# Optimization experiments

Measured on AMD Instinct MI355X. Metric: run time of the kernel, lower is better.

Reference implementation:

```python
import jax, jax.numpy as jnp
import numpy as np

B, S, H, R, N = 8, 4096, 1024, 128, 256
A_LOGIT_INIT = 6.906754778648554      # logit(0.999)
DELTA_LOG_INIT = 0.5413248546129181   # log(exp(1.0) - 1.0), softplus^-1(1.0)


def setup_inputs() -> dict:
    key = jax.random.key(0)
    ks = jax.random.split(key, 6)
    x = jax.random.normal(ks[0], (B, S, H), dtype=jnp.float32)
    state0 = jnp.zeros((B, N), dtype=jnp.float32)
    in_basis = jax.random.normal(ks[1], (R, H), dtype=jnp.float32) / np.sqrt(H)
    q_select = jax.random.normal(ks[2], (N, R), dtype=jnp.float32) / np.sqrt(R)
    k_select = jax.random.normal(ks[3], (N, R), dtype=jnp.float32) / np.sqrt(R)
    v_input = jax.random.normal(ks[4], (N, R), dtype=jnp.float32) / np.sqrt(R)
    out_proj = jax.random.normal(ks[5], (H, N), dtype=jnp.float32) / np.sqrt(N)
    a_logit = jnp.full((N,), A_LOGIT_INIT, dtype=jnp.float32)
    delta_log = jnp.full((N,), DELTA_LOG_INIT, dtype=jnp.float32)
    return {"x": x, "state0": state0, "in_basis": in_basis, "q_select": q_select,
            "k_select": k_select, "v_input": v_input, "out_proj": out_proj,
            "a_logit": a_logit, "delta_log": delta_log}


def reference(x, state0, in_basis, q_select, k_select, v_input, out_proj,
              a_logit, delta_log):
    # Projections (all timesteps at once; equivalent to per-step F.linear)
    z = jnp.einsum('bsh,rh->bsr', x, in_basis)          # [B,S,R]
    b = jnp.einsum('bsr,nr->bsn', z, k_select)          # [B,S,N]
    c = jnp.einsum('bsr,nr->bsn', z, q_select)          # [B,S,N]
    v = jnp.einsum('bsr,nr->bsn', z, v_input)           # [B,S,N]

    a = jax.nn.sigmoid(a_logit)                         # [N]
    delta = jax.nn.softplus(delta_log)                  # [N]
    u = delta * (b * v)                                 # [B,S,N] driving input

    # Diagonal linear recurrence: s_t = a * s_{t-1} + u_t ; y_t = c_t * s_t
    u_t = jnp.swapaxes(u, 0, 1)                         # [S,B,N]
    c_t = jnp.swapaxes(c, 0, 1)                         # [S,B,N]

    def step(s, inp):
        u_i, c_i = inp
        s = a * s + u_i
        return s, c_i * s

    final_state, ys = jax.lax.scan(step, state0, (u_t, c_t))  # ys: [S,B,N]
    out = jnp.einsum('sbn,hn->bsh', ys, out_proj)       # [B,S,H]
    return out, final_state
```

## Files before the change

### kernel.cpp

```cpp
#include <hip/hip_runtime.h>
#include <math.h>

#define Bb 8
#define Ss 4096
#define Hh 1024
#define Rr 128
#define Nn 256
#define Mm (Bb*Ss)
#define LCH 128
#define NCHK (Ss/LCH)

typedef __attribute__((ext_vector_type(8))) short bf16x8;
typedef __attribute__((ext_vector_type(4))) float f32x4;

__device__ __forceinline__ float sigmoidf_(float x) { return 1.0f / (1.0f + expf(-x)); }
__device__ __forceinline__ float softplusf_(float x) { return log1pf(expf(x)); }

__device__ __forceinline__ unsigned short f2b(float f) {
    union { float f; unsigned int u; } v; v.f = f;
    return (unsigned short)((v.u + 0x7fffu + ((v.u >> 16) & 1u)) >> 16);
}
__device__ __forceinline__ float b2f(unsigned short h) {
    union { unsigned int u; float f; } v; v.u = ((unsigned int)h) << 16;
    return v.f;
}

__device__ __forceinline__ void gl_lds16(const void* g, void* l) {
    __builtin_amdgcn_global_load_lds(
        (const __attribute__((address_space(1))) void*)g,
        (__attribute__((address_space(3))) void*)l, 16, 0, 0);
}


__global__ __launch_bounds__(256)
void cast_w(const float* __restrict__ s0, const float* __restrict__ s1,
            const float* __restrict__ s2, const float* __restrict__ s3,
            const float* __restrict__ s4,
            unsigned short* __restrict__ d0, unsigned short* __restrict__ d1,
            unsigned short* __restrict__ d2, unsigned short* __restrict__ d3,
            unsigned short* __restrict__ d4)
{
    const int i = blockIdx.x * 256 + threadIdx.x;
    if (i < 131072)      d0[i] = f2b(s0[i]);
    else if (i < 163840) d1[i - 131072] = f2b(s1[i - 131072]);
    else if (i < 196608) d2[i - 163840] = f2b(s2[i - 163840]);
    else if (i < 229376) d3[i - 196608] = f2b(s3[i - 196608]);
    else                 d4[i - 229376] = f2b(s4[i - 229376]);
}

__global__ __launch_bounds__(256)
void g1_fused(const float* __restrict__ X, const unsigned short* __restrict__ IB,
              unsigned short* __restrict__ Z)
{
    __shared__ __align__(16) unsigned short As[2][64 * 32];
    __shared__ __align__(16) unsigned short Bs[2][128 * 32];
    const int tid = threadIdx.x;
    const int wave = tid >> 6, lane = tid & 63;
    const int m0 = blockIdx.x * 64;
    const int wm = (wave & 1) * 32, wn = (wave >> 1) * 64;
    const int quad = lane >> 4, lm = lane & 15;
    const int srow = lane >> 2;
    const int skoff = (((lane & 3) ^ ((srow >> 1) & 3)) << 3);
    const int qsw = ((quad ^ ((lm >> 1) & 3)) << 3);
    const int arow = tid >> 3;
    const int akf = (tid & 7) * 4;
    const int awoff = ((((tid & 7) >> 1) ^ ((arow >> 1) & 3)) << 3) + (tid & 1) * 4;

    f32x4 acc[2][4] = {};
    float4 va[2];

#pragma unroll
    for (int q = 0; q < 2; ++q)
        va[q] = *(const float4*)(X + (size_t)(m0 + q * 32 + arow) * Hh + akf);
    gl_lds16(IB + (size_t)(2 * wave * 16 + srow) * Hh + skoff, &Bs[0][wave * 1024]);
    gl_lds16(IB + (size_t)((2 * wave + 1) * 16 + srow) * Hh + skoff, &Bs[0][wave * 1024 + 512]);
#pragma unroll
    for (int q = 0; q < 2; ++q) {
        uint2 o;
        o.x = (unsigned)f2b(va[q].x) | ((unsigned)f2b(va[q].y) << 16);
        o.y = (unsigned)f2b(va[q].z) | ((unsigned)f2b(va[q].w) << 16);
        *(uint2*)&As[0][(q * 32 + arow) * 32 + awoff] = o;
    }
    __syncthreads();

    int cur = 0;
    for (int k0 = 0; k0 < Hh; k0 += 32) {
        const int nxt = cur ^ 1;
        const bool more = (k0 + 32) < Hh;
        if (more) {
            gl_lds16(IB + (size_t)(2 * wave * 16 + srow) * Hh + k0 + 32 + skoff, &Bs[nxt][wave * 1024]);
            gl_lds16(IB + (size_t)((2 * wave + 1) * 16 + srow) * Hh + k0 + 32 + skoff, &Bs[nxt][wave * 1024 + 512]);
#pragma unroll
            for (int q = 0; q < 2; ++q)
                va[q] = *(const float4*)(X + (size_t)(m0 + q * 32 + arow) * Hh + k0 + 32 + akf);
        }
        bf16x8 af[2], bfv[4];
#pragma unroll
        for (int i = 0; i < 2; ++i)
            af[i] = *(const bf16x8*)&As[cur][(wm + i * 16 + lm) * 32 + qsw];
#pragma unroll
        for (int j = 0; j < 4; ++j)
            bfv[j] = *(const bf16x8*)&Bs[cur][(wn + j * 16 + lm) * 32 + qsw];
#pragma unroll
        for (int i = 0; i < 2; ++i)
#pragma unroll
            for (int j = 0; j < 4; ++j)
                acc[i][j] = __builtin_amdgcn_mfma_f32_16x16x32_bf16(af[i], bfv[j], acc[i][j], 0, 0, 0);
        if (more) {
#pragma unroll
            for (int q = 0; q < 2; ++q) {
                uint2 o;
                o.x = (unsigned)f2b(va[q].x) | ((unsigned)f2b(va[q].y) << 16);
                o.y = (unsigned)f2b(va[q].z) | ((unsigned)f2b(va[q].w) << 16);
                *(uint2*)&As[nxt][(q * 32 + arow) * 32 + awoff] = o;
            }
        }
        __syncthreads();
        cur = nxt;
    }

#pragma unroll
    for (int i = 0; i < 2; ++i) {
        const int rbase = m0 + wm + i * 16 + quad * 4;
#pragma unroll
        for (int j = 0; j < 4; ++j) {
            const int col = wn + j * 16 + lm;
#pragma unroll
            for (int r = 0; r < 4; ++r)
                Z[(size_t)(rbase + r) * Rr + col] = f2b(acc[i][j][r]);
        }
    }
}

__device__ __forceinline__ void proj_stage(const unsigned short* Zm, const unsigned short* Kw,
                                           const unsigned short* Qw, const unsigned short* Vw,
                                           char* bb, int m0, int n0, int k0,
                                           int wave, int srow, int skoff)
{
    unsigned short* zs = (unsigned short*)bb;
    unsigned short* ks = (unsigned short*)(bb + 8192);
    unsigned short* qs = (unsigned short*)(bb + 12288);
    unsigned short* vs = (unsigned short*)(bb + 16384);
    gl_lds16(Zm + (size_t)(m0 + 2 * wave * 16 + srow) * Rr + k0 + skoff, &zs[wave * 1024]);
    gl_lds16(Zm + (size_t)(m0 + (2 * wave + 1) * 16 + srow) * Rr + k0 + skoff, &zs[wave * 1024 + 512]);
    gl_lds16(Kw + (size_t)(n0 + wave * 16 + srow) * Rr + k0 + skoff, &ks[wave * 512]);
    gl_lds16(Qw + (size_t)(n0 + wave * 16 + srow) * Rr + k0 + skoff, &qs[wave * 512]);
    gl_lds16(Vw + (size_t)(n0 + wave * 16 + srow) * Rr + k0 + skoff, &vs[wave * 512]);
}

__global__ __launch_bounds__(256)
void proj_mfma(const unsigned short* __restrict__ Zm, const unsigned short* __restrict__ Kw,
               const unsigned short* __restrict__ Qw, const unsigned short* __restrict__ Vw,
               const float* __restrict__ delta_log, const float* __restrict__ a_logit,
               unsigned short* __restrict__ U, unsigned short* __restrict__ C,
               float* __restrict__ Pout)
{
    __shared__ __align__(16) char smem[41984];
    float* uL = (float*)smem;
    float* pcomb = (float*)(smem + 40960);

    const int tid = threadIdx.x;
    const int wave = tid >> 6, lane = tid & 63;
    const int m0 = blockIdx.x * 128, n0 = blockIdx.y * 64;
    const int wm = (wave & 1) * 64, wn = (wave >> 1) * 32;
    const int quad = lane >> 4, lm = lane & 15;
    const int srow = lane >> 2;
    const int skoff = (((lane & 3) ^ ((srow >> 1) & 3)) << 3);
    const int qsw = ((quad ^ ((lm >> 1) & 3)) << 3);

    f32x4 aB[4][2] = {}, aC[4][2] = {}, aV[4][2] = {};

    proj_stage(Zm, Kw, Qw, Vw, smem, m0, n0, 0, wave, srow, skoff);
    __syncthreads();

    int cur = 0;
    for (int p = 0; p < 4; ++p) {
        if (p < 3)
            proj_stage(Zm, Kw, Qw, Vw, smem + (cur ^ 1) * 20480, m0, n0,
                       (p + 1) * 32, wave, srow, skoff);
        const unsigned short* zsc = (const unsigned short*)(smem + cur * 20480);
        const unsigned short* ksc = zsc + 4096;
        const unsigned short* qsc = zsc + 6144;
        const unsigned short* vsc = zsc + 8192;
        bf16x8 zf[4], wf[2];
#pragma unroll
        for (int i = 0; i < 4; ++i)
            zf[i] = *(const bf16x8*)&zsc[(wm + i * 16 + lm) * 32 + qsw];
#pragma unroll
        for (int j = 0; j < 2; ++j)
            wf[j] = *(const bf16x8*)&ksc[(wn + j * 16 + lm) * 32 + qsw];
#pragma unroll
        for (int i = 0; i < 4; ++i)
#pragma unroll
            for (int j = 0; j < 2; ++j)
                aB[i][j] = __builtin_amdgcn_mfma_f32_16x16x32_bf16(zf[i], wf[j], aB[i][j], 0, 0, 0);
#pragma unroll
        for (int j = 0; j < 2; ++j)
            wf[j] = *(const bf16x8*)&qsc[(wn + j * 16 + lm) * 32 + qsw];
#pragma unroll
        for (int i = 0; i < 4; ++i)
#pragma unroll
            for (int j = 0; j < 2; ++j)
                aC[i][j] = __builtin_amdgcn_mfma_f32_16x16x32_bf16(zf[i], wf[j], aC[i][j], 0, 0, 0);
#pragma unroll
        for (int j = 0; j < 2; ++j)
            wf[j] = *(const bf16x8*)&vsc[(wn + j * 16 + lm) * 32 + qsw];
#pragma unroll
        for (int i = 0; i < 4; ++i)
#pragma unroll
            for (int j = 0; j < 2; ++j)
                aV[i][j] = __builtin_amdgcn_mfma_f32_16x16x32_bf16(zf[i], wf[j], aV[i][j], 0, 0, 0);
        __syncthreads();
        cur ^= 1;
    }

    float dl[2];
#pragma unroll
    for (int j = 0; j < 2; ++j)
        dl[j] = softplusf_(delta_log[n0 + wn + j * 16 + lm]);

#pragma unroll
    for (int i = 0; i < 4; ++i) {
        const int lrow = wm + i * 16 + quad * 4;
        const int rbase = m0 + lrow;
#pragma unroll
        for (int j = 0; j < 2; ++j) {
            const int col = wn + j * 16 + lm;
            const int gcol = n0 + col;
#pragma unroll
            for (int r = 0; r < 4; ++r) {
                const float uval = dl[j] * aB[i][j][r] * aV[i][j][r];
                const size_t idx = (size_t)(rbase + r) * Nn + gcol;
                U[idx] = f2b(uval);
                C[idx] = f2b(aC[i][j][r]);
                uL[(lrow + r) * 66 + col] = uval;
            }
        }
    }
    __syncthreads();

    const int colp = tid & 63, seg = tid >> 6;
    const float a = sigmoidf_(a_logit[n0 + colp]);
    float l = 0.0f;
#pragma unroll 8
    for (int r = 0; r < 32; ++r)
        l = fmaf(a, l, uL[(seg * 32 + r) * 66 + colp]);
    pcomb[seg * 64 + colp] = l;
    __syncthreads();
    if (tid < 64) {
        float a32 = a;
#pragma unroll
        for (int i = 0; i < 5; ++i) a32 *= a32;
        const float Pv = ((pcomb[tid] * a32 + pcomb[64 + tid]) * a32
                          + pcomb[128 + tid]) * a32 + pcomb[192 + tid];
        Pout[(size_t)blockIdx.x * Nn + n0 + tid] = Pv;
    }
}

__global__ __launch_bounds__(256)
void scan_mid(const float* __restrict__ P, const float* __restrict__ state0,
              const float* __restrict__ a_logit,
              float* __restrict__ start, float* __restrict__ final_state)
{
    const int g = blockIdx.x * blockDim.x + threadIdx.x;
    const int n = g & (Nn - 1);
    const int b = g >> 8;
    const float a = sigmoidf_(a_logit[n]);
    float aL = a;
#pragma unroll
    for (int i = 0; i < 7; ++i) aL *= aL;
    float s = state0[g];
#pragma unroll
    for (int ch = 0; ch < NCHK; ++ch) {
        const size_t idx = ((size_t)(b * NCHK + ch)) * Nn + n;
        start[idx] = s;
        s = fmaf(aL, s, P[idx]);
    }
    final_state[g] = s;
}

__global__ __launch_bounds__(512, 4)
void scan_g4_fused(const unsigned short* __restrict__ U, const unsigned short* __restrict__ C,
                   const float* __restrict__ start, const float* __restrict__ a_logit,
                   const unsigned short* __restrict__ OB, float* __restrict__ Out)
{
    __shared__ __align__(16) unsigned short ys[128 * 256];
    __shared__ __align__(16) unsigned short Bs[2][128 * 32];
    const int tid = threadIdx.x;
    const int wave = tid >> 6, lane = tid & 63;
    const int hbase = blockIdx.x * 512;
    const int m0 = blockIdx.y * 128;
    const int bidx = m0 >> 12;
    const int ch = (m0 & (Ss - 1)) >> 7;
    const int quad = lane >> 4, lm = lane & 15;
    const int srow = lane >> 2;
    const int skoff = (((lane & 3) ^ ((srow >> 1) & 3)) << 3);
    const int qsw = ((quad ^ ((lm >> 1) & 3)) << 3);

    if (tid < 128) {
        const int n = tid * 2;
        const float a0 = sigmoidf_(a_logit[n]);
        const float a1 = sigmoidf_(a_logit[n + 1]);
        const size_t sb = ((size_t)(bidx * NCHK + ch)) * Nn + n;
        float s0 = start[sb], s1 = start[sb + 1];
        size_t gb = ((size_t)m0) * Nn + n;
        const int slot = n >> 3;
        const int e = n & 7;
#pragma unroll 8
        for (int t = 0; t < LCH; ++t) {
            const unsigned uu = *(const unsigned*)(U + gb);
            const unsigned cc = *(const unsigned*)(C + gb);
            s0 = fmaf(a0, s0, b2f((unsigned short)uu));
            s1 = fmaf(a1, s1, b2f((unsigned short)(uu >> 16)));
            const float y0 = b2f((unsigned short)cc) * s0;
            const float y1 = b2f((unsigned short)(cc >> 16)) * s1;
            *(unsigned*)&ys[t * 256 + (((slot ^ (t & 7)) << 3) + e)] =
                (unsigned)f2b(y0) | ((unsigned)f2b(y1) << 16);
            gb += Nn;
        }
    } else if (wave >= 4) {
#pragma unroll
        for (int q = 0; q < 2; ++q) {
            const int reg = 2 * (wave - 4) + q;
            gl_lds16(OB + (size_t)(hbase + reg * 16 + srow) * Nn + skoff, &Bs[0][reg * 512]);
        }
    }
    __syncthreads();

    const int wm = (wave & 1) * 64, wn = (wave >> 1) * 32;
    f32x4 acc[4][2];

    for (int kk = 0; kk < 32; ++kk) {
        const int buf = kk & 1;
        if ((kk & 7) == 0) {
#pragma unroll
            for (int i = 0; i < 4; ++i)
#pragma unroll
                for (int j = 0; j < 2; ++j)
                    acc[i][j] = (f32x4){0.f, 0.f, 0.f, 0.f};
        }
        if (kk + 1 < 32) {
            const int n0g = hbase + ((kk + 1) >> 3) * 128;
            const int k0n = ((kk + 1) & 7) * 32;
            gl_lds16(OB + (size_t)(n0g + wave * 16 + srow) * Nn + k0n + skoff,
                     &Bs[buf ^ 1][wave * 512]);
        }
        const int k0 = (kk & 7) * 32;
        const int c8 = (k0 >> 3) + quad;
        bf16x8 af[4], bfv[2];
#pragma unroll
        for (int i = 0; i < 4; ++i) {
            const int r = wm + i * 16 + lm;
            af[i] = *(const bf16x8*)&ys[r * 256 + ((c8 ^ (r & 7)) << 3)];
        }
#pragma unroll
        for (int j = 0; j < 2; ++j)
            bfv[j] = *(const bf16x8*)&Bs[buf][(wn + j * 16 + lm) * 32 + qsw];
#pragma unroll
        for (int i = 0; i < 4; ++i)
#pragma unroll
            for (int j = 0; j < 2; ++j)
                acc[i][j] = __builtin_amdgcn_mfma_f32_16x16x32_bf16(af[i], bfv[j], acc[i][j], 0, 0, 0);
        if ((kk & 7) == 7) {
            const int n0g = hbase + (kk >> 3) * 128;
#pragma unroll
            for (int i = 0; i < 4; ++i) {
                const int rbase = m0 + wm + i * 16 + quad * 4;
#pragma unroll
                for (int j = 0; j < 2; ++j) {
                    const int col = n0g + wn + j * 16 + lm;
#pragma unroll
                    for (int r = 0; r < 4; ++r)
                        Out[(size_t)(rbase + r) * Hh + col] = acc[i][j][r];
                }
            }
        }
        __syncthreads();
    }
}

extern "C" void kernel_launch(void* const* d_in, const int* in_sizes, int n_in,
                              void* d_out, int out_size, void* d_ws, size_t ws_size,
                              hipStream_t stream)
{
    const float* x         = (const float*)d_in[0];
    const float* state0    = (const float*)d_in[1];
    const float* in_basis  = (const float*)d_in[2];
    const float* q_select  = (const float*)d_in[3];
    const float* k_select  = (const float*)d_in[4];
    const float* v_input   = (const float*)d_in[5];
    const float* out_proj  = (const float*)d_in[6];
    const float* a_logit   = (const float*)d_in[7];
    const float* delta_log = (const float*)d_in[8];

    float* out = (float*)d_out;
    float* final_state = out + (size_t)Mm * Hh;

    char* ws = (char*)d_ws;
    unsigned short* u  = (unsigned short*)ws;
    unsigned short* c  = (unsigned short*)(ws + 16777216);
    unsigned short* zb = (unsigned short*)(ws + 33554432);
    unsigned short* ib = (unsigned short*)(ws + 41943040);
    unsigned short* kb = (unsigned short*)(ws + 42205184);
    unsigned short* qb = (unsigned short*)(ws + 42270720);
    unsigned short* vb = (unsigned short*)(ws + 42336256);
    unsigned short* ob = (unsigned short*)(ws + 42401792);
    float* P  = (float*)(ws + 42926080);
    float* st = (float*)(ws + 43188224);

    cast_w<<<491520 / 256, 256, 0, stream>>>(in_basis, k_select, q_select, v_input, out_proj,
                                             ib, kb, qb, vb, ob);

    g1_fused<<<Mm / 64, 256, 0, stream>>>(x, ib, zb);

    proj_mfma<<<dim3(Mm / 128, Nn / 64), 256, 0, stream>>>(zb, kb, qb, vb,
                                                           delta_log, a_logit, u, c, P);

    scan_mid<<<(Bb * Nn) / 256, 256, 0, stream>>>(P, state0, a_logit, st, final_state);

    scan_g4_fused<<<dim3(2, Mm / 128), 512, 0, stream>>>(u, c, st, a_logit, ob, out);
}
```

Baseline: 308.5 us.

## Interleave U and C into one buffer and read out_proj directly from global

The projection kernel now writes u and c as one packed 32-bit word per element instead of two separate bf16 arrays, so the scan reads a single 8-byte vector per step instead of two scattered 4-byte loads. The output GEMM in the scan kernel drops its LDS double-buffered staging of out_proj and the per-iteration barriers, loading B fragments straight from global memory (the bf16 weights are small and likely cache-resident). This removes the syncthreads and LDS traffic but relies on L2/L1 hits and adds global-load latency inside the MFMA loop. The LDS footprint per block shrinks, which could also help occupancy.

```diff
diff --git a/kernel.cpp b/kernel.cpp
--- a/kernel.cpp
+++ b/kernel.cpp
@@ -152,8 +152,7 @@
 void proj_mfma(const unsigned short* __restrict__ Zm, const unsigned short* __restrict__ Kw,
                const unsigned short* __restrict__ Qw, const unsigned short* __restrict__ Vw,
                const float* __restrict__ delta_log, const float* __restrict__ a_logit,
-               unsigned short* __restrict__ U, unsigned short* __restrict__ C,
-               float* __restrict__ Pout)
+               unsigned int* __restrict__ UC, float* __restrict__ Pout)
 {
     __shared__ __align__(16) char smem[41984];
     float* uL = (float*)smem;
@@ -231,8 +230,7 @@
             for (int r = 0; r < 4; ++r) {
                 const float uval = dl[j] * aB[i][j][r] * aV[i][j][r];
                 const size_t idx = (size_t)(rbase + r) * Nn + gcol;
-                U[idx] = f2b(uval);
-                C[idx] = f2b(aC[i][j][r]);
+                UC[idx] = (unsigned)f2b(uval) | ((unsigned)f2b(aC[i][j][r]) << 16);
                 uL[(lrow + r) * 66 + col] = uval;
             }
         }
@@ -280,12 +278,11 @@
 }
 
 __global__ __launch_bounds__(512, 4)
-void scan_g4_fused(const unsigned short* __restrict__ U, const unsigned short* __restrict__ C,
+void scan_g4_fused(const unsigned int* __restrict__ UC,
                    const float* __restrict__ start, const float* __restrict__ a_logit,
                    const unsigned short* __restrict__ OB, float* __restrict__ Out)
 {
     __shared__ __align__(16) unsigned short ys[128 * 256];
-    __shared__ __align__(16) unsigned short Bs[2][128 * 32];
     const int tid = threadIdx.x;
     const int wave = tid >> 6, lane = tid & 63;
     const int hbase = blockIdx.x * 512;
@@ -293,9 +290,6 @@
     const int bidx = m0 >> 12;
     const int ch = (m0 & (Ss - 1)) >> 7;
     const int quad = lane >> 4, lm = lane & 15;
-    const int srow = lane >> 2;
-    const int skoff = (((lane & 3) ^ ((srow >> 1) & 3)) << 3);
-    const int qsw = ((quad ^ ((lm >> 1) & 3)) << 3);
 
     if (tid < 128) {
         const int n = tid * 2;
@@ -308,74 +302,53 @@
         const int e = n & 7;
 #pragma unroll 8
         for (int t = 0; t < LCH; ++t) {
-            const unsigned uu = *(const unsigned*)(U + gb);
-            const unsigned cc = *(const unsigned*)(C + gb);
-            s0 = fmaf(a0, s0, b2f((unsigned short)uu));
-            s1 = fmaf(a1, s1, b2f((unsigned short)(uu >> 16)));
-            const float y0 = b2f((unsigned short)cc) * s0;
-            const float y1 = b2f((unsigned short)(cc >> 16)) * s1;
+            const uint2 w = *(const uint2*)(UC + gb);
+            s0 = fmaf(a0, s0, b2f((unsigned short)(w.x & 0xffffu)));
+            s1 = fmaf(a1, s1, b2f((unsigned short)(w.y & 0xffffu)));
+            const float y0 = b2f((unsigned short)(w.x >> 16)) * s0;
+            const float y1 = b2f((unsigned short)(w.y >> 16)) * s1;
             *(unsigned*)&ys[t * 256 + (((slot ^ (t & 7)) << 3) + e)] =
                 (unsigned)f2b(y0) | ((unsigned)f2b(y1) << 16);
             gb += Nn;
         }
-    } else if (wave >= 4) {
-#pragma unroll
-        for (int q = 0; q < 2; ++q) {
-            const int reg = 2 * (wave - 4) + q;
-            gl_lds16(OB + (size_t)(hbase + reg * 16 + srow) * Nn + skoff, &Bs[0][reg * 512]);
-        }
     }
     __syncthreads();
 
     const int wm = (wave & 1) * 64, wn = (wave >> 1) * 32;
-    f32x4 acc[4][2];
-
-    for (int kk = 0; kk < 32; ++kk) {
-        const int buf = kk & 1;
-        if ((kk & 7) == 0) {
+
+    for (int sub = 0; sub < 4; ++sub) {
+        const int n0g = hbase + sub * 128;
+        f32x4 acc[4][2] = {};
+#pragma unroll 2
+        for (int p = 0; p < 8; ++p) {
+            const int k0 = p * 32;
+            bf16x8 bfv[2], af[4];
+#pragma unroll
+            for (int j = 0; j < 2; ++j)
+                bfv[j] = *(const bf16x8*)(OB + (size_t)(n0g + wn + j * 16 + lm) * Nn + k0 + quad * 8);
+            const int c8 = p * 4 + quad;
+#pragma unroll
+            for (int i = 0; i < 4; ++i) {
+                const int r = wm + i * 16 + lm;
+                af[i] = *(const bf16x8*)&ys[r * 256 + ((c8 ^ (r & 7)) << 3)];
+            }
 #pragma unroll
             for (int i = 0; i < 4; ++i)
 #pragma unroll
                 for (int j = 0; j < 2; ++j)
-                    acc[i][j] = (f32x4){0.f, 0.f, 0.f, 0.f};
-        }
-        if (kk + 1 < 32) {
-            const int n0g = hbase + ((kk + 1) >> 3) * 128;
-            const int k0n = ((kk + 1) & 7) * 32;
-            gl_lds16(OB + (size_t)(n0g + wave * 16 + srow) * Nn + k0n + skoff,
-                     &Bs[buf ^ 1][wave * 512]);
-        }
-        const int k0 = (kk & 7) * 32;
-        const int c8 = (k0 >> 3) + quad;
-        bf16x8 af[4], bfv[2];
+                    acc[i][j] = __builtin_amdgcn_mfma_f32_16x16x32_bf16(af[i], bfv[j], acc[i][j], 0, 0, 0);
+        }
 #pragma unroll
         for (int i = 0; i < 4; ++i) {
-            const int r = wm + i * 16 + lm;
-            af[i] = *(const bf16x8*)&ys[r * 256 + ((c8 ^ (r & 7)) << 3)];
-        }
-#pragma unroll
-        for (int j = 0; j < 2; ++j)
-            bfv[j] = *(const bf16x8*)&Bs[buf][(wn + j * 16 + lm) * 32 + qsw];
-#pragma unroll
-        for (int i = 0; i < 4; ++i)
-#pragma unroll
-            for (int j = 0; j < 2; ++j)
-                acc[i][j] = __builtin_amdgcn_mfma_f32_16x16x32_bf16(af[i], bfv[j], acc[i][j], 0, 0, 0);
-        if ((kk & 7) == 7) {
-            const int n0g = hbase + (kk >> 3) * 128;
-#pragma unroll
-            for (int i = 0; i < 4; ++i) {
-                const int rbase = m0 + wm + i * 16 + quad * 4;
-#pragma unroll
-                for (int j = 0; j < 2; ++j) {
-                    const int col = n0g + wn + j * 16 + lm;
-#pragma unroll
-                    for (int r = 0; r < 4; ++r)
-                        Out[(size_t)(rbase + r) * Hh + col] = acc[i][j][r];
-                }
+            const int rbase = m0 + wm + i * 16 + quad * 4;
+#pragma unroll
+            for (int j = 0; j < 2; ++j) {
+                const int col = n0g + wn + j * 16 + lm;
+#pragma unroll
+                for (int r = 0; r < 4; ++r)
+                    Out[(size_t)(rbase + r) * Hh + col] = acc[i][j][r];
             }
         }
-        __syncthreads();
     }
 }
 
@@ -397,8 +370,7 @@
     float* final_state = out + (size_t)Mm * Hh;
 
     char* ws = (char*)d_ws;
-    unsigned short* u  = (unsigned short*)ws;
-    unsigned short* c  = (unsigned short*)(ws + 16777216);
+    unsigned int* uc   = (unsigned int*)ws;
     unsigned short* zb = (unsigned short*)(ws + 33554432);
     unsigned short* ib = (unsigned short*)(ws + 41943040);
     unsigned short* kb = (unsigned short*)(ws + 42205184);
@@ -414,9 +386,9 @@
     g1_fused<<<Mm / 64, 256, 0, stream>>>(x, ib, zb);
 
     proj_mfma<<<dim3(Mm / 128, Nn / 64), 256, 0, stream>>>(zb, kb, qb, vb,
-                                                           delta_log, a_logit, u, c, P);
+                                                           delta_log, a_logit, uc, P);
 
     scan_mid<<<(Bb * Nn) / 256, 256, 0, stream>>>(P, state0, a_logit, st, final_state);
 
-    scan_g4_fused<<<dim3(2, Mm / 128), 512, 0, stream>>>(u, c, st, a_logit, ob, out);
-}
+    scan_g4_fused<<<dim3(2, Mm / 128), 512, 0, stream>>>(uc, st, a_logit, ob, out);
+}
```

After: 317.6 us. 1.03x slower.
